# Kernel optimization log

Measured on AMD Instinct MI355X. Metric: run time of the kernel, lower is better.

Reference implementation:

```python
import jax, jax.numpy as jnp
import numpy as np

B = 200
SIZES = [65536, 16384, 4096, 1024, 256, 64]
DEG = 9
LOG_SIGMA = -1000.0  # weight log-sigma init (-1000) -> sigma = exp(-1000) == 0 in fp32, deterministic sample w = mu
P_DROP = 0.1
BN_EPS = 1e-5


def setup_inputs() -> dict:
    key = jax.random.key(0)
    ks = iter(jax.random.split(key, 64))
    d = {"x": jax.random.normal(next(ks), (B, SIZES[0], 3), jnp.float32)}
    din = 3
    for l in range(5):
        nin, nout = SIZES[l], SIZES[l + 1]
        E = nout * DEG
        d[f"src{l+1}"] = jax.random.randint(next(ks), (E,), 0, nin, dtype=jnp.int32)
        d[f"dst{l+1}"] = jnp.sort(jax.random.randint(next(ks), (E,), 0, nout, dtype=jnp.int32))
        d[f"w{l+1}"] = 0.1 * jax.random.normal(next(ks), (E, din, 1), jnp.float32)
        d[f"b{l+1}"] = 0.01 * jax.random.normal(next(ks), (nout, 1), jnp.float32)
        if l < 4:
            d[f"gamma{l+1}"] = jnp.ones((nout,), jnp.float32)
            d[f"beta{l+1}"] = jnp.zeros((nout,), jnp.float32)
        din = 1
    return d


def _pool(h, src, dst, w_mu, bias, n_out):
    # Bayesian sparse pooler: w = mu + exp(LOG_SIGMA)*eps == mu (sigma underflows to 0 in fp32)
    msgs = jnp.einsum('bed,edo->beo', h[:, src], w_mu)  # (B, E, dout) gathered weighted messages
    out = jnp.zeros((h.shape[0], n_out, w_mu.shape[2]), h.dtype).at[:, dst].add(msgs) + bias
    kl = jnp.sum(0.5 * (w_mu * w_mu - 1.0) - LOG_SIGMA)  # KL(N(mu, sig^2) || N(0, 1)) per weight, summed
    return out, kl


def _bn(h, gamma, beta):
    # training-mode BatchNorm1d over (B, C, 1): batch stats per channel (biased var, as torch)
    m = h.mean(axis=0, keepdims=True)
    v = h.var(axis=0, keepdims=True)
    hn = (h - m) * jax.lax.rsqrt(v + BN_EPS)
    return hn * gamma[None, :, None] + beta[None, :, None]


def _dropout(h, k):
    keep = jax.random.bernoulli(k, 1.0 - P_DROP, h.shape)
    return jnp.where(keep, h / (1.0 - P_DROP), jnp.zeros((), h.dtype))


def reference(x, src1, dst1, w1, b1, gamma1, beta1, src2, dst2, w2, b2, gamma2, beta2, src3, dst3, w3, b3, gamma3, beta3, src4, dst4, w4, b4, gamma4, beta4, src5, dst5, w5, b5):
    dkeys = jax.random.split(jax.random.key(42), 4)
    layers = [
        (src1, dst1, w1, b1, gamma1, beta1),
        (src2, dst2, w2, b2, gamma2, beta2),
        (src3, dst3, w3, b3, gamma3, beta3),
        (src4, dst4, w4, b4, gamma4, beta4),
    ]
    h = x
    kl_tot = jnp.float32(0.0)
    for l, (s, dd, w, b, g, bt) in enumerate(layers):
        h, kl = _pool(h, s, dd, w, b, SIZES[l + 1])
        kl_tot = kl_tot + kl
        h = _dropout(jax.nn.relu(_bn(h, g, bt)), dkeys[l])
    h, kl = _pool(h, src5, dst5, w5, b5, SIZES[5])
    kl_tot = kl_tot + kl
    return h[..., 0], kl_tot  # (B, 64), scalar KL
```

## Files before the change

### kernel.cpp

```cpp
#include <hip/hip_runtime.h>
#include <hip/hip_fp16.h>
#include <stdint.h>

#define B_    200
#define N0    65536
#define COLS  (N0 * 3)
#define JT    64
#define TPAD2 228

__device__ static inline unsigned short f2h(float f) {
  __half h = __float2half(f);
  return *reinterpret_cast<unsigned short*>(&h);
}
__device__ static inline float h2f(unsigned short u) {
  __half h = *reinterpret_cast<__half*>(&u);
  return __half2float(h);
}

__host__ __device__ static inline void tf2x32(uint32_t k0, uint32_t k1,
                                              uint32_t x0, uint32_t x1,
                                              uint32_t& o0, uint32_t& o1) {
  const uint32_t ks2 = k0 ^ k1 ^ 0x1BD11BDAu;
  x0 += k0; x1 += k1;
#define TF_R(r) { x0 += x1; x1 = (x1 << (r)) | (x1 >> (32 - (r))); x1 ^= x0; }
  TF_R(13) TF_R(15) TF_R(26) TF_R(6)   x0 += k1;  x1 += ks2 + 1u;
  TF_R(17) TF_R(29) TF_R(16) TF_R(24)  x0 += ks2; x1 += k0  + 2u;
  TF_R(13) TF_R(15) TF_R(26) TF_R(6)   x0 += k0;  x1 += k1  + 3u;
  TF_R(17) TF_R(29) TF_R(16) TF_R(24)  x0 += k1;  x1 += ks2 + 4u;
  TF_R(13) TF_R(15) TF_R(26) TF_R(6)   x0 += ks2; x1 += k0  + 5u;
#undef TF_R
  o0 = x0; o1 = x1;
}

__device__ static inline float drop_mask_apply(float hn, uint32_t b, uint32_t c,
                                               uint32_t nout, uint32_t k0, uint32_t k1) {
  uint32_t o0, o1;
  tf2x32(k0, k1, 0u, b * nout + c, o0, o1);
  uint32_t bits = o0 ^ o1;
  float u = __uint_as_float((bits >> 9) | 0x3f800000u) - 1.0f;
  return (u < 0.9f) ? hn * (1.0f / 0.9f) : 0.0f;
}

__global__ void build_rp_all(const int* __restrict__ dst0, const int* __restrict__ dst1,
                             const int* __restrict__ dst2, const int* __restrict__ dst3,
                             const int* __restrict__ dst4,
                             int* rp0, int* rp1, int* rp2, int* rp3, int* rp4,
                             float* kl) {
  int tid = blockIdx.x * blockDim.x + threadIdx.x;
  if (tid == 0) *kl = 0.f;
  if (tid >= 21829) return;
  const int starts[6] = {0, 16385, 20482, 21507, 21764, 21829};
  const int EDGa[5]   = {147456, 36864, 9216, 2304, 576};
  const int* dsts[5]  = {dst0, dst1, dst2, dst3, dst4};
  int* rps[5]         = {rp0, rp1, rp2, rp3, rp4};
  int l = 0;
  while (tid >= starts[l + 1]) ++l;
  int c = tid - starts[l];
  const int* dst = dsts[l];
  int lo = 0, hi = EDGa[l];
  while (lo < hi) { int mid = (lo + hi) >> 1; if (dst[mid] < c) lo = mid + 1; else hi = mid; }
  rps[l][c] = lo;
}

__global__ __launch_bounds__(256) void kl_all_kernel(
    const float* __restrict__ w0, const float* __restrict__ w1,
    const float* __restrict__ w2, const float* __restrict__ w3,
    const float* __restrict__ w4, float* __restrict__ out) {
  __shared__ float red[256];
  const float* ws[5] = {w0, w1, w2, w3, w4};
  const int    ns[5] = {442368, 36864, 9216, 2304, 576};
  int stride = gridDim.x * blockDim.x;
  int tid0 = blockIdx.x * blockDim.x + threadIdx.x;
  float s = 0.f;
#pragma unroll
  for (int l = 0; l < 5; ++l) {
    const float* w = ws[l];
    int n = ns[l];
    for (int i = tid0; i < n; i += stride) {
      float v = w[i];
      s += fmaf(0.5f * v, v, 999.5f);
    }
  }
  red[threadIdx.x] = s;
  __syncthreads();
  for (int st = 128; st > 0; st >>= 1) {
    if (threadIdx.x < st) red[threadIdx.x] += red[threadIdx.x + st];
    __syncthreads();
  }
  if (threadIdx.x == 0) atomicAdd(out, red[0]);
}

__global__ __launch_bounds__(512, 4) void transpose_rows_kernel(
    const float* __restrict__ x, unsigned short* __restrict__ xT2) {
  __shared__ unsigned short tile[JT * TPAD2];
  const int t  = threadIdx.x;
  const int nb = COLS / JT;
  const int bid = (int)blockIdx.x;
  const int sb  = (bid & 7) * (nb >> 3) + (bid >> 3);
  const int j0 = sb * JT;
  const int tx = t & 15;
  const int bl = t >> 4;

  const float* xp = x + j0 + (tx << 2);
  float4 v[7];
#pragma unroll
  for (int p = 0; p < 7; ++p) {
    int b = bl + (p << 5);
    b = b < B_ ? b : B_ - 1;
    v[p] = *(const float4*)(xp + (size_t)b * COLS);
  }
  __builtin_amdgcn_sched_barrier(0);
#pragma unroll
  for (int p = 0; p < 7; ++p) {
    int b = bl + (p << 5);
    if (b < B_) {
      int base = (tx << 2) * TPAD2 + b;
      tile[base            ] = f2h(v[p].x);
      tile[base +     TPAD2] = f2h(v[p].y);
      tile[base + 2 * TPAD2] = f2h(v[p].z);
      tile[base + 3 * TPAD2] = f2h(v[p].w);
    }
  }
  __syncthreads();
#pragma unroll
  for (int q = 0; q < 7; ++q) {
    unsigned idx = (unsigned)t + ((unsigned)q << 9);
    if (idx < 3200u) {
      unsigned row = idx / 50u;
      unsigned g   = idx - row * 50u;
      uint2 o = *(const uint2*)&tile[row * TPAD2 + (g << 2)];
      *(uint2*)(xT2 + (size_t)(j0 + row) * B_ + (g << 2)) = o;
    }
  }
}

__global__ __launch_bounds__(256) void pool1_bn_wave(
    const unsigned short* __restrict__ xT2, const int* __restrict__ src,
    const float* __restrict__ w, const float* __restrict__ bias,
    const int* __restrict__ rp, const float* __restrict__ gamma,
    const float* __restrict__ beta, unsigned short* __restrict__ out,
    uint32_t k0, uint32_t k1) {
  __shared__ float part[2][64][4];
  const int l    = threadIdx.x & 63;
  const int wid  = threadIdx.x >> 6;
  const int chl  = wid & 1;
  const int half = wid >> 1;
  const int c    = ((int)blockIdx.x << 1) + chl;
  const bool act = (l < 50);
  const int b4   = (act ? l : 0) << 2;

  float a0 = 0.f, a1 = 0.f, a2 = 0.f, a3 = 0.f;
  const int e1 = rp[c + 1];
  int e = rp[c] + half;
#define P1_EDGE(EE)                                                          \
  {                                                                          \
    const unsigned short* base = xT2 + (size_t)src[EE] * (3 * B_) + b4;      \
    float w0 = w[3 * (EE)], w1 = w[3 * (EE) + 1], w2 = w[3 * (EE) + 2];      \
    uint2 p0 = *(const uint2*)(base);                                        \
    uint2 p1 = *(const uint2*)(base + B_);                                   \
    uint2 p2 = *(const uint2*)(base + 2 * B_);                               \
    a0 = fmaf(h2f((unsigned short)p0.x), w0, a0);                            \
    a1 = fmaf(h2f((unsigned short)(p0.x >> 16)), w0, a1);                    \
    a2 = fmaf(h2f((unsigned short)p0.y), w0, a2);                            \
    a3 = fmaf(h2f((unsigned short)(p0.y >> 16)), w0, a3);                    \
    a0 = fmaf(h2f((unsigned short)p1.x), w1, a0);                            \
    a1 = fmaf(h2f((unsigned short)(p1.x >> 16)), w1, a1);                    \
    a2 = fmaf(h2f((unsigned short)p1.y), w1, a2);                            \
    a3 = fmaf(h2f((unsigned short)(p1.y >> 16)), w1, a3);                    \
    a0 = fmaf(h2f((unsigned short)p2.x), w2, a0);                            \
    a1 = fmaf(h2f((unsigned short)(p2.x >> 16)), w2, a1);                    \
    a2 = fmaf(h2f((unsigned short)p2.y), w2, a2);                            \
    a3 = fmaf(h2f((unsigned short)(p2.y >> 16)), w2, a3);                    \
  }
  for (; e + 2 < e1; e += 4) { P1_EDGE(e) P1_EDGE(e + 2) }
  for (; e < e1; e += 2) { P1_EDGE(e) }
#undef P1_EDGE

  if (half == 1) {
    part[chl][l][0] = a0; part[chl][l][1] = a1;
    part[chl][l][2] = a2; part[chl][l][3] = a3;
  }
  __syncthreads();
  if (half == 1) return;
  a0 += part[chl][l][0]; a1 += part[chl][l][1];
  a2 += part[chl][l][2]; a3 += part[chl][l][3];
  const float bi = bias[c];
  a0 += bi; a1 += bi; a2 += bi; a3 += bi;
  if (!act) { a0 = a1 = a2 = a3 = 0.f; }

  float sv = a0 + a1 + a2 + a3;
  float qv = a0 * a0 + a1 * a1 + a2 * a2 + a3 * a3;
#pragma unroll
  for (int off = 32; off; off >>= 1) {
    sv += __shfl_xor(sv, off);
    qv += __shfl_xor(qv, off);
  }
  const float m   = sv * (1.f / 200.f);
  const float var = fmaf(qv, 1.f / 200.f, -m * m);
  const float scale = gamma[c] * rsqrtf(var + 1e-5f);
  const float shift = fmaf(-m, scale, beta[c]);

  if (act) {
    float r0 = drop_mask_apply(fmaxf(fmaf(a0, scale, shift), 0.f), (uint32_t)b4,      (uint32_t)c, 16384u, k0, k1);
    float r1 = drop_mask_apply(fmaxf(fmaf(a1, scale, shift), 0.f), (uint32_t)b4 + 1u, (uint32_t)c, 16384u, k0, k1);
    float r2 = drop_mask_apply(fmaxf(fmaf(a2, scale, shift), 0.f), (uint32_t)b4 + 2u, (uint32_t)c, 16384u, k0, k1);
    float r3 = drop_mask_apply(fmaxf(fmaf(a3, scale, shift), 0.f), (uint32_t)b4 + 3u, (uint32_t)c, 16384u, k0, k1);
    uint2 pk;
    pk.x = (uint32_t)f2h(r0) | ((uint32_t)f2h(r1) << 16);
    pk.y = (uint32_t)f2h(r2) | ((uint32_t)f2h(r3) << 16);
    *(uint2*)(out + (size_t)c * B_ + b4) = pk;
  }
}

__global__ __launch_bounds__(256) void pooln_wave(
    const unsigned short* __restrict__ hin, const int* __restrict__ src,
    const float* __restrict__ w, const float* __restrict__ bias,
    const int* __restrict__ rp, const float* __restrict__ gamma,
    const float* __restrict__ beta, void* __restrict__ outv,
    int nout, int has_bn, uint32_t k0, uint32_t k1) {
  __shared__ float part[2][64][4];
  const int l    = threadIdx.x & 63;
  const int wid  = threadIdx.x >> 6;
  const int chl  = wid & 1;
  const int half = wid >> 1;
  const int c    = ((int)blockIdx.x << 1) + chl;
  const bool act = (l < 50);
  const int b4   = (act ? l : 0) << 2;

  float a0 = 0.f, a1 = 0.f, a2 = 0.f, a3 = 0.f;
  const int e1 = rp[c + 1];
  int e = rp[c] + half;
#define PN_EDGE(EE)                                                          \
  {                                                                          \
    const unsigned short* base = hin + (size_t)src[EE] * B_ + b4;            \
    float we = w[EE];                                                        \
    uint2 p0 = *(const uint2*)(base);                                        \
    a0 = fmaf(h2f((unsigned short)p0.x), we, a0);                            \
    a1 = fmaf(h2f((unsigned short)(p0.x >> 16)), we, a1);                    \
    a2 = fmaf(h2f((unsigned short)p0.y), we, a2);                            \
    a3 = fmaf(h2f((unsigned short)(p0.y >> 16)), we, a3);                    \
  }
  for (; e + 2 < e1; e += 4) { PN_EDGE(e) PN_EDGE(e + 2) }
  for (; e < e1; e += 2) { PN_EDGE(e) }
#undef PN_EDGE

  if (half == 1) {
    part[chl][l][0] = a0; part[chl][l][1] = a1;
    part[chl][l][2] = a2; part[chl][l][3] = a3;
  }
  __syncthreads();
  if (half == 1) return;
  a0 += part[chl][l][0]; a1 += part[chl][l][1];
  a2 += part[chl][l][2]; a3 += part[chl][l][3];
  const float bi = bias[c];
  a0 += bi; a1 += bi; a2 += bi; a3 += bi;

  if (has_bn) {
    if (!act) { a0 = a1 = a2 = a3 = 0.f; }
    float sv = a0 + a1 + a2 + a3;
    float qv = a0 * a0 + a1 * a1 + a2 * a2 + a3 * a3;
#pragma unroll
    for (int off = 32; off; off >>= 1) {
      sv += __shfl_xor(sv, off);
      qv += __shfl_xor(qv, off);
    }
    const float m   = sv * (1.f / 200.f);
    const float var = fmaf(qv, 1.f / 200.f, -m * m);
    const float scale = gamma[c] * rsqrtf(var + 1e-5f);
    const float shift = fmaf(-m, scale, beta[c]);
    if (act) {
      unsigned short* out = (unsigned short*)outv;
      uint32_t no = (uint32_t)nout;
      float r0 = drop_mask_apply(fmaxf(fmaf(a0, scale, shift), 0.f), (uint32_t)b4,      (uint32_t)c, no, k0, k1);
      float r1 = drop_mask_apply(fmaxf(fmaf(a1, scale, shift), 0.f), (uint32_t)b4 + 1u, (uint32_t)c, no, k0, k1);
      float r2 = drop_mask_apply(fmaxf(fmaf(a2, scale, shift), 0.f), (uint32_t)b4 + 2u, (uint32_t)c, no, k0, k1);
      float r3 = drop_mask_apply(fmaxf(fmaf(a3, scale, shift), 0.f), (uint32_t)b4 + 3u, (uint32_t)c, no, k0, k1);
      uint2 pk;
      pk.x = (uint32_t)f2h(r0) | ((uint32_t)f2h(r1) << 16);
      pk.y = (uint32_t)f2h(r2) | ((uint32_t)f2h(r3) << 16);
      *(uint2*)(out + (size_t)c * B_ + b4) = pk;
    }
  } else if (act) {
    float* out = (float*)outv;
    out[(size_t)(b4    ) * 64 + c] = a0;
    out[(size_t)(b4 + 1) * 64 + c] = a1;
    out[(size_t)(b4 + 2) * 64 + c] = a2;
    out[(size_t)(b4 + 3) * 64 + c] = a3;
  }
}

extern "C" void kernel_launch(void* const* d_in, const int* in_sizes, int n_in,
                              void* d_out, int out_size, void* d_ws, size_t ws_size,
                              hipStream_t stream) {
  (void)in_sizes; (void)n_in; (void)out_size; (void)ws_size;
  const float* x = (const float*)d_in[0];
  const int*   src[5]; const int* dst[5];
  const float* w[5];   const float* bias[5];
  const float* gamma[4]; const float* beta[4];
  int idx = 1;
  for (int l = 0; l < 5; ++l) {
    src[l]  = (const int*)d_in[idx++];
    dst[l]  = (const int*)d_in[idx++];
    w[l]    = (const float*)d_in[idx++];
    bias[l] = (const float*)d_in[idx++];
    if (l < 4) { gamma[l] = (const float*)d_in[idx++]; beta[l] = (const float*)d_in[idx++]; }
  }
  static const int NOUT[5] = {16384, 4096, 1024, 256, 64};

  uint32_t dk0[4], dk1[4];
  for (uint32_t i = 0; i < 4; ++i) tf2x32(0u, 42u, 0u, i, dk0[i], dk1[i]);

  char* ws = (char*)d_ws;
  size_t off = 0;
  auto carve = [&](size_t bytes) -> void* {
    void* p = ws + off;
    off = (off + bytes + 255) & ~(size_t)255;
    return p;
  };
  int* rp[5];
  for (int l = 0; l < 5; ++l) rp[l] = (int*)carve((size_t)(NOUT[l] + 1) * sizeof(int));
  unsigned short* h1 = (unsigned short*)carve((size_t)16384 * B_ * 2);
  unsigned short* h2 = (unsigned short*)carve((size_t)4096 * B_ * 2);
  unsigned short* h3 = (unsigned short*)carve((size_t)1024 * B_ * 2);
  unsigned short* h4 = (unsigned short*)carve((size_t)256 * B_ * 2);
  unsigned short* xT2 = (unsigned short*)carve((size_t)COLS * B_ * 2);

  float* kl = (float*)d_out + 12800;

  build_rp_all<<<(21829 + 255) / 256, 256, 0, stream>>>(
      dst[0], dst[1], dst[2], dst[3], dst[4],
      rp[0], rp[1], rp[2], rp[3], rp[4], kl);

  kl_all_kernel<<<256, 256, 0, stream>>>(w[0], w[1], w[2], w[3], w[4], kl);

  transpose_rows_kernel<<<COLS / JT, 512, 0, stream>>>(x, xT2);

  pool1_bn_wave<<<16384 / 2, 256, 0, stream>>>(
      xT2, src[0], w[0], bias[0], rp[0], gamma[0], beta[0], h1,
      dk0[0], dk1[0]);

  pooln_wave<<<4096 / 2, 256, 0, stream>>>(
      h1, src[1], w[1], bias[1], rp[1], gamma[1], beta[1], h2, 4096, 1,
      dk0[1], dk1[1]);
  pooln_wave<<<1024 / 2, 256, 0, stream>>>(
      h2, src[2], w[2], bias[2], rp[2], gamma[2], beta[2], h3, 1024, 1,
      dk0[2], dk1[2]);
  pooln_wave<<<256 / 2, 256, 0, stream>>>(
      h3, src[3], w[3], bias[3], rp[3], gamma[3], beta[3], h4, 256, 1,
      dk0[3], dk1[3]);
  pooln_wave<<<64 / 2, 256, 0, stream>>>(
      h4, src[4], w[4], bias[4], rp[4], nullptr, nullptr, (float*)d_out, 64, 0,
      0u, 0u);
}
```

Baseline: 111.0 us.

## Merge row-pointer, KL and transpose kernels into one launch with inline-asm loads

Folds the CSR row-pointer build and the KL reduction into extra blocks of the transpose kernel, so three launches become one, plus a memset that zeroes the KL accumulator. The transpose loads are rewritten as inline assembly that issues seven dwordx4 global loads back to back before one wait, replacing the compiler-scheduled loop. The aim is to cut launch overhead and let the small auxiliary work overlap the bandwidth-bound transpose. The trade-offs are a kernel whose blocks do unrelated work and a hand-written load sequence the compiler cannot reschedule.

```diff
diff --git a/kernel.cpp b/kernel.cpp
--- a/kernel.cpp
+++ b/kernel.cpp
@@ -7,6 +7,12 @@
 #define COLS  (N0 * 3)
 #define JT    64
 #define TPAD2 228
+
+#define NTB   (COLS / JT)
+#define RPB   43
+#define KLB   64
+
+typedef float f32x4 __attribute__((ext_vector_type(4)));
 
 __device__ static inline unsigned short f2h(float f) {
   __half h = __float2half(f);
@@ -41,85 +47,109 @@
   return (u < 0.9f) ? hn * (1.0f / 0.9f) : 0.0f;
 }
 
-__global__ void build_rp_all(const int* __restrict__ dst0, const int* __restrict__ dst1,
-                             const int* __restrict__ dst2, const int* __restrict__ dst3,
-                             const int* __restrict__ dst4,
-                             int* rp0, int* rp1, int* rp2, int* rp3, int* rp4,
-                             float* kl) {
-  int tid = blockIdx.x * blockDim.x + threadIdx.x;
-  if (tid == 0) *kl = 0.f;
-  if (tid >= 21829) return;
-  const int starts[6] = {0, 16385, 20482, 21507, 21764, 21829};
-  const int EDGa[5]   = {147456, 36864, 9216, 2304, 576};
-  const int* dsts[5]  = {dst0, dst1, dst2, dst3, dst4};
-  int* rps[5]         = {rp0, rp1, rp2, rp3, rp4};
-  int l = 0;
-  while (tid >= starts[l + 1]) ++l;
-  int c = tid - starts[l];
-  const int* dst = dsts[l];
-  int lo = 0, hi = EDGa[l];
-  while (lo < hi) { int mid = (lo + hi) >> 1; if (dst[mid] < c) lo = mid + 1; else hi = mid; }
-  rps[l][c] = lo;
-}
-
-__global__ __launch_bounds__(256) void kl_all_kernel(
+__global__ __launch_bounds__(512, 4) void transpose_aux_kernel(
+    const float* __restrict__ x, unsigned short* __restrict__ xT2,
+    const int* __restrict__ dst0, const int* __restrict__ dst1,
+    const int* __restrict__ dst2, const int* __restrict__ dst3,
+    const int* __restrict__ dst4,
+    int* __restrict__ rp0, int* __restrict__ rp1, int* __restrict__ rp2,
+    int* __restrict__ rp3, int* __restrict__ rp4,
     const float* __restrict__ w0, const float* __restrict__ w1,
     const float* __restrict__ w2, const float* __restrict__ w3,
-    const float* __restrict__ w4, float* __restrict__ out) {
-  __shared__ float red[256];
-  const float* ws[5] = {w0, w1, w2, w3, w4};
-  const int    ns[5] = {442368, 36864, 9216, 2304, 576};
-  int stride = gridDim.x * blockDim.x;
-  int tid0 = blockIdx.x * blockDim.x + threadIdx.x;
-  float s = 0.f;
+    const float* __restrict__ w4, float* __restrict__ kl) {
+  __shared__ unsigned short tile[JT * TPAD2];
+  const int bid = (int)blockIdx.x;
+  const int t   = threadIdx.x;
+
+  if (bid >= NTB) {
+    if (bid < NTB + RPB) {
+      int tid = (bid - NTB) * 512 + t;
+      if (tid >= 21829) return;
+      const int starts[6] = {0, 16385, 20482, 21507, 21764, 21829};
+      const int EDGa[5]   = {147456, 36864, 9216, 2304, 576};
+      const int* dsts[5]  = {dst0, dst1, dst2, dst3, dst4};
+      int* rps[5]         = {rp0, rp1, rp2, rp3, rp4};
+      int l = 0;
+      while (tid >= starts[l + 1]) ++l;
+      int c = tid - starts[l];
+      const int* dst = dsts[l];
+      int lo = 0, hi = EDGa[l];
+      while (lo < hi) { int mid = (lo + hi) >> 1; if (dst[mid] < c) lo = mid + 1; else hi = mid; }
+      rps[l][c] = lo;
+    } else {
+      float* red = (float*)tile;
+      const float* ws[5] = {w0, w1, w2, w3, w4};
+      const int    ns[5] = {442368, 36864, 9216, 2304, 576};
+      const int stride = KLB * 512;
+      const int tid0 = (bid - NTB - RPB) * 512 + t;
+      float s = 0.f;
 #pragma unroll
-  for (int l = 0; l < 5; ++l) {
-    const float* w = ws[l];
-    int n = ns[l];
-    for (int i = tid0; i < n; i += stride) {
-      float v = w[i];
-      s += fmaf(0.5f * v, v, 999.5f);
-    }
-  }
-  red[threadIdx.x] = s;
-  __syncthreads();
-  for (int st = 128; st > 0; st >>= 1) {
-    if (threadIdx.x < st) red[threadIdx.x] += red[threadIdx.x + st];
-    __syncthreads();
-  }
-  if (threadIdx.x == 0) atomicAdd(out, red[0]);
-}
-
-__global__ __launch_bounds__(512, 4) void transpose_rows_kernel(
-    const float* __restrict__ x, unsigned short* __restrict__ xT2) {
-  __shared__ unsigned short tile[JT * TPAD2];
-  const int t  = threadIdx.x;
-  const int nb = COLS / JT;
-  const int bid = (int)blockIdx.x;
-  const int sb  = (bid & 7) * (nb >> 3) + (bid >> 3);
+      for (int l = 0; l < 5; ++l) {
+        const float* w = ws[l];
+        int n = ns[l];
+        for (int i = tid0; i < n; i += stride) {
+          float v = w[i];
+          s += fmaf(0.5f * v, v, 999.5f);
+        }
+      }
+      red[t] = s;
+      __syncthreads();
+      for (int st = 256; st > 0; st >>= 1) {
+        if (t < st) red[t] += red[t + st];
+        __syncthreads();
+      }
+      if (t == 0) atomicAdd(kl, red[0]);
+    }
+    return;
+  }
+
+  const int sb = (bid & 7) * (NTB >> 3) + (bid >> 3);
   const int j0 = sb * JT;
   const int tx = t & 15;
   const int bl = t >> 4;
 
   const float* xp = x + j0 + (tx << 2);
-  float4 v[7];
-#pragma unroll
-  for (int p = 0; p < 7; ++p) {
-    int b = bl + (p << 5);
-    b = b < B_ ? b : B_ - 1;
-    v[p] = *(const float4*)(xp + (size_t)b * COLS);
-  }
-  __builtin_amdgcn_sched_barrier(0);
-#pragma unroll
-  for (int p = 0; p < 7; ++p) {
-    int b = bl + (p << 5);
-    if (b < B_) {
-      int base = (tx << 2) * TPAD2 + b;
-      tile[base            ] = f2h(v[p].x);
-      tile[base +     TPAD2] = f2h(v[p].y);
-      tile[base + 2 * TPAD2] = f2h(v[p].z);
-      tile[base + 3 * TPAD2] = f2h(v[p].w);
-    }
+  const float* a0 = xp + (size_t)(bl      ) * COLS;
+  const float* a1 = xp + (size_t)(bl +  32) * COLS;
+  const float* a2 = xp + (size_t)(bl +  64) * COLS;
+  const float* a3 = xp + (size_t)(bl +  96) * COLS;
+  const float* a4 = xp + (size_t)(bl + 128) * COLS;
+  const float* a5 = xp + (size_t)(bl + 160) * COLS;
+  const int b6 = (bl + 192 < B_) ? bl + 192 : B_ - 1;
+  const float* a6 = xp + (size_t)b6 * COLS;
+
+  f32x4 v0, v1, v2, v3, v4, v5, v6;
+  asm volatile(
+      "global_load_dwordx4 %0, %7, off\n\t"
+      "global_load_dwordx4 %1, %8, off\n\t"
+      "global_load_dwordx4 %2, %9, off\n\t"
+      "global_load_dwordx4 %3, %10, off\n\t"
+      "global_load_dwordx4 %4, %11, off\n\t"
+      "global_load_dwordx4 %5, %12, off\n\t"
+      "global_load_dwordx4 %6, %13, off\n\t"
+      "s_waitcnt vmcnt(0)"
+      : "=&v"(v0), "=&v"(v1), "=&v"(v2), "=&v"(v3), "=&v"(v4), "=&v"(v5), "=&v"(v6)
+      : "v"(a0), "v"(a1), "v"(a2), "v"(a3), "v"(a4), "v"(a5), "v"(a6)
+      : "memory");
+
+  {
+    const int base = (tx << 2) * TPAD2;
+#define ST_ROW(VV, BB)                                                      \
+    {                                                                       \
+      int o = base + (BB);                                                  \
+      tile[o            ] = f2h((VV)[0]);                                   \
+      tile[o +     TPAD2] = f2h((VV)[1]);                                   \
+      tile[o + 2 * TPAD2] = f2h((VV)[2]);                                   \
+      tile[o + 3 * TPAD2] = f2h((VV)[3]);                                   \
+    }
+    ST_ROW(v0, bl)
+    ST_ROW(v1, bl + 32)
+    ST_ROW(v2, bl + 64)
+    ST_ROW(v3, bl + 96)
+    ST_ROW(v4, bl + 128)
+    ST_ROW(v5, bl + 160)
+    if (bl < 8) ST_ROW(v6, bl + 192)
+#undef ST_ROW
   }
   __syncthreads();
 #pragma unroll
@@ -327,13 +357,13 @@
 
   float* kl = (float*)d_out + 12800;
 
-  build_rp_all<<<(21829 + 255) / 256, 256, 0, stream>>>(
+  hipMemsetAsync(kl, 0, sizeof(float), stream);
+
+  transpose_aux_kernel<<<NTB + RPB + KLB, 512, 0, stream>>>(
+      x, xT2,
       dst[0], dst[1], dst[2], dst[3], dst[4],
-      rp[0], rp[1], rp[2], rp[3], rp[4], kl);
-
-  kl_all_kernel<<<256, 256, 0, stream>>>(w[0], w[1], w[2], w[3], w[4], kl);
-
-  transpose_rows_kernel<<<COLS / JT, 512, 0, stream>>>(x, xT2);
+      rp[0], rp[1], rp[2], rp[3], rp[4],
+      w[0], w[1], w[2], w[3], w[4], kl);
 
   pool1_bn_wave<<<16384 / 2, 256, 0, stream>>>(
       xT2, src[0], w[0], bias[0], rp[0], gamma[0], beta[0], h1,
```

After: 105.9 us. -4.6%, faster.
